# Kernel optimization log

Measured on AMD Instinct MI355X. Metric: run time of the kernel, lower is better.

Reference implementation:

```python
import jax, jax.numpy as jnp
import numpy as np

B, T_K, SENT_T_K, N = 16, 2048, 64, 512  # N = 2*hidden_dim


def setup_inputs() -> dict:
    key = jax.random.key(0)
    ks = jax.random.split(key, 12)
    f = lambda k, shape: jax.random.normal(k, shape, dtype=jnp.float32)
    # sentence end positions: 64 sentences of 32 tokens each (strictly increasing, last == T_K)
    end = (jnp.arange(1, SENT_T_K + 1) * (T_K // SENT_T_K)).astype(jnp.int32)
    enc_sent_pos = jnp.tile(end[None, :], (B, 1))
    return {
        "s_t_hat": f(ks[0], (B, N)),
        "enc_sent_pos": enc_sent_pos,
        "encoder_outputs": f(ks[1], (B, T_K, N)),
        "encoder_feature": f(ks[2], (B * T_K, N)),
        "enc_padding_mask": jnp.ones((B, T_K), jnp.float32),
        "sent_s_t_hat": f(ks[3], (B, N)),
        "sent_enc_outputs": f(ks[4], (B, SENT_T_K, N)),
        "sent_enc_feature": f(ks[5], (B * SENT_T_K, N)),
        "sent_enc_padding_mask": jnp.ones((B, SENT_T_K), jnp.float32),
        "coverage": jax.random.uniform(ks[6], (B, T_K), dtype=jnp.float32),
        # learned params
        "W_dec": f(ks[7], (N, N)) * 0.02,
        "b_dec": jnp.zeros((N,), jnp.float32),
        "v_w": f(ks[8], (N,)) * 0.02,
        "W_sent_dec": f(ks[9], (N, N)) * 0.02,
        "b_sent_dec": jnp.zeros((N,), jnp.float32),
        "sent_v_w": f(ks[10], (N,)) * 0.02,
        "w_c": f(ks[11], (N,)) * 0.02,  # W_c: Linear(1, N, bias=False)
    }


def _attend(s, enc_out, enc_feat, mask, W, bvec, v, extra):
    b, t, n = enc_out.shape
    dec = s @ W.T + bvec                                    # [b, n]
    e = jnp.tanh(enc_feat.reshape(b, t, n) + dec[:, None, :] + extra)
    scores = jnp.einsum('btn,n->bt', e, v)                  # v: Linear(n, 1, bias=False)
    a = jax.nn.softmax(scores, axis=1) * mask
    a = a / a.sum(axis=1, keepdims=True)
    c = jnp.einsum('bt,btn->bn', a, enc_out)
    return c, a


def reference(s_t_hat, enc_sent_pos, encoder_outputs, encoder_feature, enc_padding_mask,
              sent_s_t_hat, sent_enc_outputs, sent_enc_feature, sent_enc_padding_mask,
              coverage, W_dec, b_dec, v_w, W_sent_dec, b_sent_dec, sent_v_w, w_c):
    b, t_k, n = encoder_outputs.shape
    sent_t_k = sent_enc_outputs.shape[1]

    # word-level Bahdanau attention with coverage feature (W_c on coverage scalar)
    cov_feat = coverage[:, :, None] * w_c                   # [b, t_k, n]
    c_t, attn_dist = _attend(s_t_hat, encoder_outputs, encoder_feature,
                             enc_padding_mask, W_dec, b_dec, v_w, cov_feat)

    # sentence-level attention
    sent_c_t, sent_attn_dist = _attend(sent_s_t_hat, sent_enc_outputs, sent_enc_feature,
                                       sent_enc_padding_mask, W_sent_dec, b_sent_dec,
                                       sent_v_w, 0.0)

    # ragged per-sentence renormalization (replaces the nested python loop):
    # seg[bi, t] = number of end_ids <= t  == sentence index of token t
    pos = jnp.arange(t_k)
    seg = jax.vmap(lambda e: jnp.searchsorted(e, pos, side='right'))(enc_sent_pos)  # [b, t_k]
    valid = seg < sent_t_k                                   # tokens past last end id untouched (stay 0)
    segc = jnp.minimum(seg, sent_t_k - 1)
    seg_sums = jax.vmap(lambda a, s: jax.ops.segment_sum(a, s, num_segments=SENT_T_K))(
        jnp.where(valid, attn_dist, 0.0), segc)              # [b, sent_t_k]
    per_tok_sum = jnp.take_along_axis(seg_sums, segc, axis=1)
    per_tok_sent = jnp.take_along_axis(sent_attn_dist, segc, axis=1)
    attn_dist_sw = jnp.where(valid, attn_dist / per_tok_sum * per_tok_sent, 0.0)

    coverage_new = coverage + attn_dist_sw                   # is_coverage branch
    return (c_t, attn_dist, coverage_new, sent_c_t, sent_attn_dist)
```

## Files before the change

kernel.cpp:

```cpp
#include <hip/hip_runtime.h>

#define BB 16
#define T_K 2048
#define SENT_T 64
#define NN 512
#define WORD_ROWS (BB * T_K)
#define SENT_ROWS (BB * SENT_T)

__device__ __forceinline__ float fast_tanh(float x) {
    return 1.f - 2.f / (1.f + __expf(2.f * x));
}

__global__ __launch_bounds__(256) void dec_fused(
    const float* __restrict__ s_w, const float* __restrict__ W_w, const float* __restrict__ bias_w,
    const float* __restrict__ s_s, const float* __restrict__ W_s, const float* __restrict__ bias_s,
    float* __restrict__ dec, float* __restrict__ sdec)
{
    int blk = blockIdx.x;
    int b = blk & (BB - 1);
    bool sent = blk >= BB;
    const float* s    = sent ? s_s   : s_w;
    const float* W    = sent ? W_s   : W_w;
    const float* bias = sent ? bias_s : bias_w;
    float* out        = sent ? sdec  : dec;

    __shared__ float sv[NN];
    for (int i = threadIdx.x; i < NN; i += 256) sv[i] = s[b * NN + i];
    __syncthreads();
    for (int n = threadIdx.x; n < NN; n += 256) {
        const float4* Wr = reinterpret_cast<const float4*>(W + (size_t)n * NN);
        float acc = 0.f;
#pragma unroll 8
        for (int k = 0; k < NN / 4; ++k) {
            float4 w4 = Wr[k];
            acc = fmaf(w4.x, sv[4 * k + 0], acc);
            acc = fmaf(w4.y, sv[4 * k + 1], acc);
            acc = fmaf(w4.z, sv[4 * k + 2], acc);
            acc = fmaf(w4.w, sv[4 * k + 3], acc);
        }
        out[b * NN + n] = acc + bias[n];
    }
}

__global__ __launch_bounds__(256) void scores_all(
    const float* __restrict__ feat,  const float* __restrict__ dec,
    const float* __restrict__ v,     const float* __restrict__ wc,
    const float* __restrict__ cov,
    const float* __restrict__ sfeat, const float* __restrict__ sdec,
    const float* __restrict__ sv_,
    float* __restrict__ wscores, float* __restrict__ sscores)
{
    int gw = (blockIdx.x * 256 + threadIdx.x) >> 6;
    int lane = threadIdx.x & 63;
    bool word = gw < WORD_ROWS;
    int row = word ? gw : gw - WORD_ROWS;
    int b = word ? (row >> 11) : (row >> 6);

    const float4* f4 = reinterpret_cast<const float4*>((word ? feat : sfeat) + (size_t)row * NN);
    const float4* d4 = reinterpret_cast<const float4*>((word ? dec : sdec) + (size_t)b * NN);
    const float4* v4 = reinterpret_cast<const float4*>(word ? v : sv_);
    const float4* w4 = reinterpret_cast<const float4*>(wc);
    float c = word ? cov[row] : 0.f;

    float acc = 0.f;
#pragma unroll
    for (int i = 0; i < 2; ++i) {
        int idx = lane + 64 * i;
        float4 f = f4[idx];
        float4 d = d4[idx];
        float4 vv = v4[idx];
        float ex = 0.f, ey = 0.f, ez = 0.f, ew = 0.f;
        if (word) {
            float4 w = w4[idx];
            ex = c * w.x; ey = c * w.y; ez = c * w.z; ew = c * w.w;
        }
        acc += vv.x * fast_tanh(f.x + d.x + ex);
        acc += vv.y * fast_tanh(f.y + d.y + ey);
        acc += vv.z * fast_tanh(f.z + d.z + ez);
        acc += vv.w * fast_tanh(f.w + d.w + ew);
    }
    for (int off = 32; off; off >>= 1) acc += __shfl_down(acc, off, 64);
    if (lane == 0) {
        if (word) wscores[row] = acc;
        else      sscores[row] = acc;
    }
}

__global__ __launch_bounds__(256) void mid_kernel(
    float* __restrict__ attn,
    const float* __restrict__ mask,
    float* __restrict__ sattn,
    const float* __restrict__ smask,
    const float* __restrict__ senc,
    float* __restrict__ sct,
    const int* __restrict__ pos,
    const float* __restrict__ cov,
    float* __restrict__ cov_out,
    float* __restrict__ ct)
{
    int b = blockIdx.x, tid = threadIdx.x;
    int wid = tid >> 6, lane = tid & 63;
    __shared__ float sa[SENT_T];
    __shared__ float ssum[SENT_T];
    __shared__ int ends[SENT_T];
    __shared__ float redm[4], reds[4], red2[4];

    ct[b * NN + tid] = 0.f;
    ct[b * NN + tid + 256] = 0.f;

    if (tid < SENT_T) {
        float s = sattn[b * SENT_T + tid];
        float m = s;
        for (int off = 32; off; off >>= 1) m = fmaxf(m, __shfl_xor(m, off, 64));
        float p = __expf(s - m);
        float sum = p;
        for (int off = 32; off; off >>= 1) sum += __shfl_xor(sum, off, 64);
        float a0 = p / sum * smask[b * SENT_T + tid];
        float s2 = a0;
        for (int off = 32; off; off >>= 1) s2 += __shfl_xor(s2, off, 64);
        float a = a0 / s2;
        sattn[b * SENT_T + tid] = a;
        sa[tid] = a;
        ends[tid] = pos[b * SENT_T + tid];
        ssum[tid] = 0.f;
    }

    const int base = b * T_K + tid * 8;
    float4 v0 = *reinterpret_cast<const float4*>(attn + base);
    float4 v1 = *reinterpret_cast<const float4*>(attn + base + 4);
    float vv[8] = {v0.x, v0.y, v0.z, v0.w, v1.x, v1.y, v1.z, v1.w};

    float m = vv[0];
#pragma unroll
    for (int i = 1; i < 8; ++i) m = fmaxf(m, vv[i]);
    for (int off = 32; off; off >>= 1) m = fmaxf(m, __shfl_xor(m, off, 64));
    if (lane == 0) redm[wid] = m;
    __syncthreads();
    m = fmaxf(fmaxf(redm[0], redm[1]), fmaxf(redm[2], redm[3]));

    float p[8], s = 0.f;
#pragma unroll
    for (int i = 0; i < 8; ++i) { p[i] = __expf(vv[i] - m); s += p[i]; }
    for (int off = 32; off; off >>= 1) s += __shfl_xor(s, off, 64);
    if (lane == 0) reds[wid] = s;
    __syncthreads();
    s = reds[0] + reds[1] + reds[2] + reds[3];

    float4 m0 = *reinterpret_cast<const float4*>(mask + base);
    float4 m1 = *reinterpret_cast<const float4*>(mask + base + 4);
    float mk[8] = {m0.x, m0.y, m0.z, m0.w, m1.x, m1.y, m1.z, m1.w};
    float a0[8], s2 = 0.f;
#pragma unroll
    for (int i = 0; i < 8; ++i) { a0[i] = p[i] / s * mk[i]; s2 += a0[i]; }
    for (int off = 32; off; off >>= 1) s2 += __shfl_xor(s2, off, 64);
    if (lane == 0) red2[wid] = s2;
    __syncthreads();
    s2 = red2[0] + red2[1] + red2[2] + red2[3];
    float r = 1.f / s2;

    float a[8];
    int seg[8];
#pragma unroll
    for (int i = 0; i < 8; ++i) {
        a[i] = a0[i] * r;
        int t = tid * 8 + i;
        int lo = 0, hi = SENT_T;
        while (lo < hi) { int mid = (lo + hi) >> 1; if (ends[mid] <= t) lo = mid + 1; else hi = mid; }
        seg[i] = lo;
        if (lo < SENT_T) atomicAdd(&ssum[lo], a[i]);
    }
    float4 o0 = {a[0], a[1], a[2], a[3]};
    float4 o1 = {a[4], a[5], a[6], a[7]};
    *reinterpret_cast<float4*>(attn + base) = o0;
    *reinterpret_cast<float4*>(attn + base + 4) = o1;
    __syncthreads();

    float4 c0 = *reinterpret_cast<const float4*>(cov + base);
    float4 c1 = *reinterpret_cast<const float4*>(cov + base + 4);
    float cvv[8] = {c0.x, c0.y, c0.z, c0.w, c1.x, c1.y, c1.z, c1.w};
    float co[8];
#pragma unroll
    for (int i = 0; i < 8; ++i) {
        float sw = 0.f;
        if (seg[i] < SENT_T) sw = a[i] / ssum[seg[i]] * sa[seg[i]];
        co[i] = cvv[i] + sw;
    }
    float4 q0 = {co[0], co[1], co[2], co[3]};
    float4 q1 = {co[4], co[5], co[6], co[7]};
    *reinterpret_cast<float4*>(cov_out + base) = q0;
    *reinterpret_cast<float4*>(cov_out + base + 4) = q1;

    for (int n = tid; n < NN; n += 256) {
        float acc = 0.f;
#pragma unroll 8
        for (int t = 0; t < SENT_T; ++t)
            acc = fmaf(sa[t], senc[((size_t)b * SENT_T + t) * NN + n], acc);
        sct[b * NN + n] = acc;
    }
}

__global__ __launch_bounds__(256) void ct_kernel(
    const float* __restrict__ attn,
    const float* __restrict__ enc,
    float* __restrict__ ct)
{
    int b = blockIdx.y, chunk = blockIdx.x, tid = threadIdx.x;
    __shared__ float a_sh[64];
    if (tid < 64) a_sh[tid] = attn[b * T_K + chunk * 64 + tid];
    __syncthreads();
    int p  = tid >> 7;
    int c4 = tid & 127;
    const float4* base = reinterpret_cast<const float4*>(enc + ((size_t)b * T_K + (size_t)chunk * 64) * NN);
    float4 acc = {0.f, 0.f, 0.f, 0.f};
#pragma unroll 8
    for (int t = 0; t < 64; t += 2) {
        int rrow = t + p;
        float av = a_sh[rrow];
        float4 e = base[rrow * (NN / 4) + c4];
        acc.x = fmaf(av, e.x, acc.x);
        acc.y = fmaf(av, e.y, acc.y);
        acc.z = fmaf(av, e.z, acc.z);
        acc.w = fmaf(av, e.w, acc.w);
    }
    float* dst = ct + b * NN + c4 * 4;
    atomicAdd(dst + 0, acc.x);
    atomicAdd(dst + 1, acc.y);
    atomicAdd(dst + 2, acc.z);
    atomicAdd(dst + 3, acc.w);
}

extern "C" void kernel_launch(void* const* d_in, const int* in_sizes, int n_in,
                              void* d_out, int out_size, void* d_ws, size_t ws_size,
                              hipStream_t stream) {
    const float* s_t_hat          = (const float*)d_in[0];
    const int*   enc_sent_pos     = (const int*)d_in[1];
    const float* encoder_outputs  = (const float*)d_in[2];
    const float* encoder_feature  = (const float*)d_in[3];
    const float* enc_padding_mask = (const float*)d_in[4];
    const float* sent_s_t_hat     = (const float*)d_in[5];
    const float* sent_enc_outputs = (const float*)d_in[6];
    const float* sent_enc_feature = (const float*)d_in[7];
    const float* sent_enc_padding_mask = (const float*)d_in[8];
    const float* coverage         = (const float*)d_in[9];
    const float* W_dec            = (const float*)d_in[10];
    const float* b_dec            = (const float*)d_in[11];
    const float* v_w              = (const float*)d_in[12];
    const float* W_sent_dec       = (const float*)d_in[13];
    const float* b_sent_dec       = (const float*)d_in[14];
    const float* sent_v_w         = (const float*)d_in[15];
    const float* w_c              = (const float*)d_in[16];

    float* out         = (float*)d_out;
    float* c_t         = out;
    float* attn_dist   = out + 8192;
    float* coverage_nw = out + 8192 + 32768;
    float* sent_c_t    = out + 8192 + 65536;
    float* sent_attn   = out + 16384 + 65536;

    float* ws   = (float*)d_ws;
    float* dec  = ws;
    float* sdec = ws + BB * NN;

    dec_fused<<<2 * BB, 256, 0, stream>>>(s_t_hat, W_dec, b_dec,
                                          sent_s_t_hat, W_sent_dec, b_sent_dec,
                                          dec, sdec);

    scores_all<<<(WORD_ROWS + SENT_ROWS) / 4, 256, 0, stream>>>(
        encoder_feature, dec, v_w, w_c, coverage,
        sent_enc_feature, sdec, sent_v_w,
        attn_dist, sent_attn);

    mid_kernel<<<BB, 256, 0, stream>>>(attn_dist, enc_padding_mask,
                                       sent_attn, sent_enc_padding_mask,
                                       sent_enc_outputs, sent_c_t,
                                       enc_sent_pos, coverage, coverage_nw, c_t);

    ct_kernel<<<dim3(T_K / 64, BB), 256, 0, stream>>>(attn_dist, encoder_outputs, c_t);
}
```

Measured before the change: 240.1 us.

## Parallelize decoder projection across blocks and move sentence context into ct kernel

The decoder projection kernel goes from 32 blocks to 256. Each block computes 64 output rows with a 4-way split over K and a shared-memory reduction, so the weight reads are spread across far more CUs. The sentence context-vector computation moves out of the 16-block mid kernel into an extra block column of the ct kernel, where it runs in parallel with the word context blocks. fast_tanh now uses the hardware reciprocal instead of a division, which slightly changes precision.

```diff
diff --git a/kernel.cpp b/kernel.cpp
--- a/kernel.cpp
+++ b/kernel.cpp
@@ -8,7 +8,8 @@
 #define SENT_ROWS (BB * SENT_T)
 
 __device__ __forceinline__ float fast_tanh(float x) {
-    return 1.f - 2.f / (1.f + __expf(2.f * x));
+    float e = __expf(2.f * x);
+    return 1.f - 2.f * __builtin_amdgcn_rcpf(1.f + e);
 }
 
 __global__ __launch_bounds__(256) void dec_fused(
@@ -17,28 +18,39 @@
     float* __restrict__ dec, float* __restrict__ sdec)
 {
     int blk = blockIdx.x;
-    int b = blk & (BB - 1);
-    bool sent = blk >= BB;
-    const float* s    = sent ? s_s   : s_w;
-    const float* W    = sent ? W_s   : W_w;
+    bool sent = blk >= 128;
+    int sub = blk & 127;
+    int b = sub >> 3;
+    int n0 = (sub & 7) * 64;
+    const float* s    = sent ? s_s    : s_w;
+    const float* W    = sent ? W_s    : W_w;
     const float* bias = sent ? bias_s : bias_w;
-    float* out        = sent ? sdec  : dec;
+    float* out        = sent ? sdec   : dec;
 
     __shared__ float sv[NN];
+    __shared__ float part[4][64];
     for (int i = threadIdx.x; i < NN; i += 256) sv[i] = s[b * NN + i];
     __syncthreads();
-    for (int n = threadIdx.x; n < NN; n += 256) {
-        const float4* Wr = reinterpret_cast<const float4*>(W + (size_t)n * NN);
-        float acc = 0.f;
-#pragma unroll 8
-        for (int k = 0; k < NN / 4; ++k) {
-            float4 w4 = Wr[k];
-            acc = fmaf(w4.x, sv[4 * k + 0], acc);
-            acc = fmaf(w4.y, sv[4 * k + 1], acc);
-            acc = fmaf(w4.z, sv[4 * k + 2], acc);
-            acc = fmaf(w4.w, sv[4 * k + 3], acc);
-        }
-        out[b * NN + n] = acc + bias[n];
+
+    int kq  = threadIdx.x >> 6;
+    int row = threadIdx.x & 63;
+    const float4* Wr  = reinterpret_cast<const float4*>(W + (size_t)(n0 + row) * NN) + kq * 32;
+    const float*  svq = sv + kq * 128;
+    float acc = 0.f;
+#pragma unroll
+    for (int j = 0; j < 32; ++j) {
+        float4 w4 = Wr[j];
+        acc = fmaf(w4.x, svq[4 * j + 0], acc);
+        acc = fmaf(w4.y, svq[4 * j + 1], acc);
+        acc = fmaf(w4.z, svq[4 * j + 2], acc);
+        acc = fmaf(w4.w, svq[4 * j + 3], acc);
+    }
+    part[kq][row] = acc;
+    __syncthreads();
+    if (threadIdx.x < 64) {
+        float r = part[0][threadIdx.x] + part[1][threadIdx.x]
+                + part[2][threadIdx.x] + part[3][threadIdx.x] + bias[n0 + threadIdx.x];
+        out[b * NN + n0 + threadIdx.x] = r;
     }
 }
 
@@ -91,8 +103,6 @@
     const float* __restrict__ mask,
     float* __restrict__ sattn,
     const float* __restrict__ smask,
-    const float* __restrict__ senc,
-    float* __restrict__ sct,
     const int* __restrict__ pos,
     const float* __restrict__ cov,
     float* __restrict__ cov_out,
@@ -189,22 +199,34 @@
     float4 q1 = {co[4], co[5], co[6], co[7]};
     *reinterpret_cast<float4*>(cov_out + base) = q0;
     *reinterpret_cast<float4*>(cov_out + base + 4) = q1;
-
-    for (int n = tid; n < NN; n += 256) {
-        float acc = 0.f;
-#pragma unroll 8
-        for (int t = 0; t < SENT_T; ++t)
-            acc = fmaf(sa[t], senc[((size_t)b * SENT_T + t) * NN + n], acc);
-        sct[b * NN + n] = acc;
-    }
 }
 
 __global__ __launch_bounds__(256) void ct_kernel(
     const float* __restrict__ attn,
     const float* __restrict__ enc,
-    float* __restrict__ ct)
+    const float* __restrict__ sattn,
+    const float* __restrict__ senc,
+    float* __restrict__ ct,
+    float* __restrict__ sct)
 {
-    int b = blockIdx.y, chunk = blockIdx.x, tid = threadIdx.x;
+    int b = blockIdx.y, tid = threadIdx.x;
+    if (blockIdx.x == 32) {
+        __shared__ float sa_sh[SENT_T];
+        if (tid < SENT_T) sa_sh[tid] = sattn[b * SENT_T + tid];
+        __syncthreads();
+        const float* basep = senc + (size_t)b * SENT_T * NN;
+        float acc0 = 0.f, acc1 = 0.f;
+#pragma unroll 8
+        for (int t = 0; t < SENT_T; ++t) {
+            float av = sa_sh[t];
+            acc0 = fmaf(av, basep[t * NN + tid], acc0);
+            acc1 = fmaf(av, basep[t * NN + tid + 256], acc1);
+        }
+        sct[b * NN + tid] = acc0;
+        sct[b * NN + tid + 256] = acc1;
+        return;
+    }
+    int chunk = blockIdx.x;
     __shared__ float a_sh[64];
     if (tid < 64) a_sh[tid] = attn[b * T_K + chunk * 64 + tid];
     __syncthreads();
@@ -261,9 +283,9 @@
     float* dec  = ws;
     float* sdec = ws + BB * NN;
 
-    dec_fused<<<2 * BB, 256, 0, stream>>>(s_t_hat, W_dec, b_dec,
-                                          sent_s_t_hat, W_sent_dec, b_sent_dec,
-                                          dec, sdec);
+    dec_fused<<<256, 256, 0, stream>>>(s_t_hat, W_dec, b_dec,
+                                       sent_s_t_hat, W_sent_dec, b_sent_dec,
+                                       dec, sdec);
 
     scores_all<<<(WORD_ROWS + SENT_ROWS) / 4, 256, 0, stream>>>(
         encoder_feature, dec, v_w, w_c, coverage,
@@ -272,8 +294,9 @@
 
     mid_kernel<<<BB, 256, 0, stream>>>(attn_dist, enc_padding_mask,
                                        sent_attn, sent_enc_padding_mask,
-                                       sent_enc_outputs, sent_c_t,
                                        enc_sent_pos, coverage, coverage_nw, c_t);
 
-    ct_kernel<<<dim3(T_K / 64, BB), 256, 0, stream>>>(attn_dist, encoder_outputs, c_t);
-}
+    ct_kernel<<<dim3(33, BB), 256, 0, stream>>>(attn_dist, encoder_outputs,
+                                                sent_attn, sent_enc_outputs,
+                                                c_t, sent_c_t);
+}
```

Result: faster. 208.1 us (-13.3%).
